# Kernel tuning notes

Hardware: AMD Instinct MI355X
Metric: run time of the kernel (lower is better)

The kernel has to match this reference:

```python
import math
import jax, jax.numpy as jnp
import numpy as np

NUM_HEADS = 16
TAU_RCS, LAMBDA_RCS = 2.0, 0.6
PATCH = 16
PREFIX = 8
GAUSS_STD = 5.0


def gaussian_window(d1, d2, std):
    c = 1.0 / (std * math.sqrt(2.0))
    k1 = (jnp.arange(d1, dtype=jnp.float32) - (d1 - 1) / 2.0) * c
    k2 = (jnp.arange(d2, dtype=jnp.float32) - (d2 - 1) / 2.0) * c
    return jnp.exp(-(k1[:, None] ** 2 + k2[None, :] ** 2))  # [d1, d2]


def attention_addition(d1, d2, prefix, std):
    # out[(a,b),(c,d)] = window[a-c+d1-1, b-d+d2-1]  (conv of delta images with window)
    win = gaussian_window(2 * d1 - 1, 2 * d2 - 1, std)
    ia = jnp.arange(d1)
    jb = jnp.arange(d2)
    r = ia[:, None] - ia[None, :] + (d1 - 1)   # [d1, d1]
    s = jb[:, None] - jb[None, :] + (d2 - 1)   # [d2, d2]
    add = win[r[:, None, :, None], s[None, :, None, :]]  # [d1,d2,d1,d2]
    add = add.reshape(d1 * d2, d1 * d2)
    add = jnp.pad(add, ((prefix, 0), (prefix, 0)))  # zero rows/cols for prefix tokens
    return add[None]  # [1, N, N]


def setup_inputs() -> dict:
    key = jax.random.key(0)
    ks = jax.random.split(key, 5)
    B, C = 4, 1024
    d1 = d2 = 512 // PATCH  # 32
    N = d1 * d2 + PREFIX    # 1032
    H = NUM_HEADS
    x = jax.random.normal(ks[0], (B, N, C), dtype=jnp.float32)
    qkv_w = jax.random.normal(ks[1], (3 * C, C), dtype=jnp.float32) * 0.02
    qkv_b = jnp.zeros((3 * C,), dtype=jnp.float32)
    proj_w = jax.random.normal(ks[2], (C, C), dtype=jnp.float32) * 0.02
    proj_b = jnp.zeros((C,), dtype=jnp.float32)
    attn_add = attention_addition(d1, d2, PREFIX, GAUSS_STD)
    # stored RCS attention maps are softmax outputs -> row-normalized positives
    rcs = jax.random.uniform(ks[3], (B * H, N, N), dtype=jnp.float32)
    rcs = rcs / jnp.sum(rcs, axis=-1, keepdims=True)
    return {"x": x, "qkv_w": qkv_w, "qkv_b": qkv_b, "proj_w": proj_w,
            "proj_b": proj_b, "attn_addition": attn_add, "rcs_attn": rcs}


def reference(x, qkv_w, qkv_b, proj_w, proj_b, attn_addition, rcs_attn):
    B, N, C = x.shape
    H = NUM_HEADS
    hd = C // H
    scale = hd ** -0.5
    qkv = jnp.einsum('bnc,dc->bnd', x, qkv_w) + qkv_b  # [B,N,3C]
    q, k, v = jnp.split(qkv, 3, axis=-1)
    def to_heads(t):
        return t.reshape(B, N, H, hd).transpose(0, 2, 1, 3).reshape(B * H, N, hd)
    k = to_heads(k)
    v = to_heads(v)
    # custom K-K attention with additive Gaussian bias
    attn = jnp.einsum('bnd,bmd->bnm', k, k) * scale + attn_addition
    attn = jax.nn.softmax(attn, axis=-1)
    # RCS blending with stored intermediate attention maps
    attn = TAU_RCS * ((1.0 - LAMBDA_RCS) * attn + LAMBDA_RCS * rcs_attn)
    out = jnp.einsum('bnm,bmd->bnd', attn, v)  # [B*H, N, hd]
    out = out.reshape(B, H, N, hd).transpose(0, 2, 1, 3).reshape(B, N, C)
    out = jnp.einsum('bnc,dc->bnd', out, proj_w) + proj_b
    return out
```

## Files before the change

kernel.cpp:

```cpp
#include <hip/hip_runtime.h>
#include <stdint.h>

#define NSEQ 1032
#define CDIM 1024
#define HD 64
#define H_HEADS 16
#define BROWS 4128
#define SCALE 0.125f

typedef __attribute__((ext_vector_type(8))) short bf16x8;
typedef __attribute__((ext_vector_type(4))) float f32x4;

__device__ __forceinline__ unsigned short f2bf(float f) {
  union { float f; uint32_t u; } c; c.f = f;
  uint32_t u = c.u;
  return (unsigned short)((u + 0x7fffu + ((u >> 16) & 1u)) >> 16);
}

__device__ __forceinline__ void gl16(const void* gp, void* lp) {
  __builtin_amdgcn_global_load_lds((const __attribute__((address_space(1))) void*)gp,
                                   (__attribute__((address_space(3))) void*)lp, 16, 0, 0);
}

__global__ void convert_f32_bf16(const float* __restrict__ src, unsigned short* __restrict__ dst, int n4) {
  int i = blockIdx.x * blockDim.x + threadIdx.x;
  if (i >= n4) return;
  float4 v = ((const float4*)src)[i];
  ushort4 o;
  o.x = f2bf(v.x); o.y = f2bf(v.y); o.z = f2bf(v.z); o.w = f2bf(v.w);
  ((ushort4*)dst)[i] = o;
}

template<int MODE>
__global__ __launch_bounds__(256, 2) void gemm_bt(
    const unsigned short* __restrict__ A,
    const unsigned short* __restrict__ Bw,
    const float* __restrict__ bias,
    unsigned short* __restrict__ outK,
    unsigned short* __restrict__ outV,
    float* __restrict__ outF,
    int M, int K)
{
  __shared__ unsigned short As[128 * 32];
  __shared__ unsigned short Bs[128 * 32];
  const int t = threadIdx.x;
  const int w = t >> 6, lane = t & 63, lr = lane & 15, lg = lane >> 4;
  const int wr = w >> 1, wc = w & 1;
  const int NXB = (MODE == 0) ? 16 : 8;
  const int cpx = gridDim.x >> 3;
  const int swz = (blockIdx.x & 7) * cpx + (blockIdx.x >> 3);
  const int m0 = (swz / NXB) * 128, n0 = (swz % NXB) * 128;
  f32x4 acc[4][4] = {};

  for (int ks = 0; ks < K; ks += 32) {
    #pragma unroll
    for (int q = 0; q < 2; ++q) {
      const int o = t + (q << 8);
      const int row = o >> 2, kc = o & 3;
      int ra = m0 + row; ra = ra < M ? ra : M - 1;
      gl16(A + (size_t)ra * K + ks + kc * 8, (void*)(As + o * 8));
      gl16(Bw + (size_t)(n0 + row) * K + ks + kc * 8, (void*)(Bs + o * 8));
    }
    __syncthreads();
    bf16x8 af[4], bfr[4];
    #pragma unroll
    for (int m = 0; m < 4; ++m)
      af[m] = *(const bf16x8*)(As + (wr * 64 + m * 16 + lr) * 32 + lg * 8);
    #pragma unroll
    for (int n = 0; n < 4; ++n)
      bfr[n] = *(const bf16x8*)(Bs + (wc * 64 + n * 16 + lr) * 32 + lg * 8);
    #pragma unroll
    for (int m = 0; m < 4; ++m)
      #pragma unroll
      for (int n = 0; n < 4; ++n)
        acc[m][n] = __builtin_amdgcn_mfma_f32_16x16x32_bf16(af[m], bfr[n], acc[m][n], 0, 0, 0);
    __syncthreads();
  }

  #pragma unroll
  for (int m = 0; m < 4; ++m) {
    const int rowb = m0 + wr * 64 + m * 16 + lg * 4;
    #pragma unroll
    for (int n = 0; n < 4; ++n) {
      const int col = n0 + wc * 64 + n * 16 + lr;
      const float bv = bias[col];
      #pragma unroll
      for (int r = 0; r < 4; ++r) {
        const int row = rowb + r;
        if (row >= M) continue;
        const float v = acc[m][n][r] + bv;
        if (MODE == 0) {
          const int b = row / NSEQ, nn = row - b * NSEQ;
          if (col < CDIM) {
            const int h = col >> 6, d = col & 63;
            outK[((size_t)(b * H_HEADS + h) * NSEQ + nn) * HD + d] = f2bf(v);
          } else {
            const int jj = col - CDIM, h = jj >> 6, d = jj & 63;
            outV[((size_t)(b * H_HEADS + h) * HD + d) * NSEQ + nn] = f2bf(v);
          }
        } else {
          outF[(size_t)row * CDIM + col] = v;
        }
      }
    }
  }
}

__global__ __launch_bounds__(256, 3) void attn_fused(
    const unsigned short* __restrict__ Kb,
    const unsigned short* __restrict__ Vt,
    const float* __restrict__ rcs,
    unsigned short* __restrict__ outp)
{
  __shared__ __align__(16) unsigned short Kc[2][64 * 64];
  __shared__ __align__(16) unsigned short Vs[2][64 * 64];
  __shared__ __align__(16) unsigned short Asm[64 * 72];
  __shared__ unsigned short Ps[64 * 72];
  const int t = threadIdx.x;
  const int w = t >> 6, lane = t & 63, lr = lane & 15, lg = lane >> 4;
  const int bid = blockIdx.x;
  const int nb = (bid & 7) * 136 + (bid >> 3);
  const int bh = nb / 17, rt = nb - bh * 17;
  const int i_base = rt * 64 + w * 16;
  const int arow = w * 16 + lr;
  const float* rbase = rcs + (size_t)bh * NSEQ * NSEQ;
  const unsigned short* kbase = Kb + (size_t)bh * NSEQ * HD;
  const unsigned short* vbase = Vt + (size_t)bh * HD * NSEQ;

  const unsigned short* srck[2]; int dok[2];
  const unsigned short* srcv[2]; int dov[2];
  #pragma unroll
  for (int q = 0; q < 2; ++q) {
    const int p = t + (q << 8);
    const int row = p >> 3, sch = p & 7;
    const int gch = (sch ^ row) & 7;
    srck[q] = kbase + (size_t)row * HD + gch * 8;  dok[q] = p * 8;
    srcv[q] = vbase + (size_t)row * NSEQ + gch * 8; dov[q] = p * 8;
  }
  auto stage_kv = [&](int tB, int buf) {
    #pragma unroll
    for (int q = 0; q < 2; ++q) gl16(srck[q] + (size_t)tB * HD, (void*)(Kc[buf] + dok[q]));
    #pragma unroll
    for (int q = 0; q < 2; ++q) gl16(srcv[q] + tB, (void*)(Vs[buf] + dov[q]));
  };
  auto stage_kv_tail = [&](int buf) {
    const int tB = 1024;
    #pragma unroll
    for (int q = 0; q < 2; ++q) {
      const int p = t + (q << 8);
      const int row = p >> 3, sch = p & 7;
      const int gch = (sch ^ row) & 7;
      int mrow = tB + row; if (mrow > NSEQ - 1) mrow = NSEQ - 1;
      gl16(kbase + (size_t)mrow * HD + gch * 8, (void*)(Kc[buf] + p * 8));
    }
    #pragma unroll
    for (int q = 0; q < 2; ++q) {
      const int p = t + (q << 8);
      const int row = p >> 3, sch = p & 7;
      const int gch = (sch ^ row) & 7;
      int gc = tB + gch * 8; if (gc > NSEQ - 8) gc = NSEQ - 8;
      gl16(vbase + (size_t)row * NSEQ + gc, (void*)(Vs[buf] + p * 8));
    }
  };

  const int ccol = (lane & 15) * 4;
  const float* rsrc[4]; int lrow_loc[4];
  #pragma unroll
  for (int j = 0; j < 4; ++j) {
    lrow_loc[j] = w * 16 + j * 4 + (lane >> 4);
    int grow = rt * 64 + lrow_loc[j]; if (grow > NSEQ - 1) grow = NSEQ - 1;
    rsrc[j] = rbase + (size_t)grow * NSEQ;
  }
  f32x4 rreg[4];
  auto ld_rcs = [&](int tB) {
    int gcol = tB + ccol; if (gcol > NSEQ - 4) gcol = NSEQ - 4;
    #pragma unroll
    for (int j = 0; j < 4; ++j) rreg[j] = *(const f32x4*)(rsrc[j] + gcol);
  };
  auto wr_rcs = [&]() {
    #pragma unroll
    for (int j = 0; j < 4; ++j) {
      ushort4 o;
      o.x = f2bf(rreg[j][0]); o.y = f2bf(rreg[j][1]);
      o.z = f2bf(rreg[j][2]); o.w = f2bf(rreg[j][3]);
      *(ushort4*)(Asm + lrow_loc[j] * 72 + ccol) = o;
    }
  };

  bf16x8 akr[2];
  {
    int row = i_base + lr; if (row > NSEQ - 1) row = NSEQ - 1;
    const unsigned short* p = kbase + (size_t)row * HD + lg * 8;
    akr[0] = *(const bf16x8*)(p);
    akr[1] = *(const bf16x8*)(p + 32);
  }

  const int irow_base = i_base + lg * 4;
  float u[16], v[16];
  #pragma unroll
  for (int fn = 0; fn < 4; ++fn) {
    const int x = 16 * fn + lr;
    const int m1_0 = ((x + 24) >> 5) - 1;
    const int m2 = (x - 8) & 31;
    #pragma unroll
    for (int r = 0; r < 4; ++r) {
      const int irow = irow_base + r;
      const int ip = irow - 8;
      const int i1 = ip >> 5, j1 = ip & 31;
      const int di = i1 - m1_0, dj = j1 - m2;
      const float iok = (irow >= 8) ? 1.f : 0.f;
      u[fn * 4 + r] = __expf(-0.02f * (float)(di * di + dj * dj)) * iok;
      v[fn * 4 + r] = __expf(0.08f * (float)di);
    }
  }
  const float C1 = 0.92311634639f;
  const float C2 = 0.85214378896f;

  f32x4 accP[4] = {};
  f32x4 accR[4] = {};
  float lsum[4] = {0.f, 0.f, 0.f, 0.f};

  ld_rcs(0);
  stage_kv(0, 0);
  wr_rcs();
  asm volatile("s_waitcnt vmcnt(0)");
  __builtin_amdgcn_s_barrier();
  __builtin_amdgcn_sched_barrier(0);

  for (int mt = 0; mt < 17; ++mt) {
    const int mB = mt * 64;
    const int cur = mt & 1, nxt = cur ^ 1;

    if (mt < 16)       ld_rcs(mB + 64);
    if (mt < 15)       stage_kv(mB + 64, nxt);
    else if (mt == 15) stage_kv_tail(nxt);

    const unsigned short* kc = Kc[cur];
    const unsigned short* vsb = Vs[cur];

    __builtin_amdgcn_s_setprio(1);
    f32x4 s[4];
    #pragma unroll
    for (int fn = 0; fn < 4; ++fn) {
      const int row = 16 * fn + lr;
      const int r7 = row & 7;
      f32x4 z = {0.f, 0.f, 0.f, 0.f};
      bf16x8 b0 = *(const bf16x8*)(kc + row * 64 + ((lg ^ r7) & 7) * 8);
      bf16x8 b1 = *(const bf16x8*)(kc + row * 64 + (((4 + lg) ^ r7) & 7) * 8);
      z = __builtin_amdgcn_mfma_f32_16x16x32_bf16(akr[0], b0, z, 0, 0, 0);
      z = __builtin_amdgcn_mfma_f32_16x16x32_bf16(akr[1], b1, z, 0, 0, 0);
      s[fn] = z;
    }
    __builtin_amdgcn_s_setprio(0);

    #pragma unroll
    for (int fn = 0; fn < 4; ++fn) {
      const int mcol = mB + 16 * fn + lr;
      const float mok = (mcol >= 8 && mcol < NSEQ) ? 1.f : 0.f;
      const bool mlt = (mcol < NSEQ);
      #pragma unroll
      for (int r = 0; r < 4; ++r) {
        const int fi = fn * 4 + r;
        const float sv = s[fn][r] * SCALE + u[fi] * mok;
        const float p = mlt ? __expf(sv) : 0.f;
        lsum[r] += p;
        Ps[(w * 16 + lg * 4 + r) * 72 + 16 * fn + lr] = f2bf(p);
        u[fi] *= v[fi] * C1;
        v[fi] *= C2;
      }
    }

    bf16x8 af[2];
    #pragma unroll
    for (int kf = 0; kf < 2; ++kf) {
      const int kg = mB + kf * 32 + lg * 8;
      if (kg + 8 <= NSEQ) {
        af[kf] = *(const bf16x8*)(Asm + arow * 72 + kf * 32 + lg * 8);
      } else {
        #pragma unroll
        for (int j = 0; j < 8; ++j) af[kf][j] = 0;
      }
    }

    bf16x8 pa0 = *(const bf16x8*)(Ps + (w * 16 + lr) * 72 + lg * 8);
    bf16x8 pa1 = *(const bf16x8*)(Ps + (w * 16 + lr) * 72 + 32 + lg * 8);
    __builtin_amdgcn_s_setprio(1);
    #pragma unroll
    for (int fd = 0; fd < 4; ++fd) {
      const int row = 16 * fd + lr;
      const int r7 = row & 7;
      bf16x8 v0 = *(const bf16x8*)(vsb + row * 64 + ((lg ^ r7) & 7) * 8);
      bf16x8 v1 = *(const bf16x8*)(vsb + row * 64 + (((4 + lg) ^ r7) & 7) * 8);
      accP[fd] = __builtin_amdgcn_mfma_f32_16x16x32_bf16(pa0, v0, accP[fd], 0, 0, 0);
      accP[fd] = __builtin_amdgcn_mfma_f32_16x16x32_bf16(pa1, v1, accP[fd], 0, 0, 0);
      accR[fd] = __builtin_amdgcn_mfma_f32_16x16x32_bf16(af[0], v0, accR[fd], 0, 0, 0);
      accR[fd] = __builtin_amdgcn_mfma_f32_16x16x32_bf16(af[1], v1, accR[fd], 0, 0, 0);
    }
    __builtin_amdgcn_s_setprio(0);

    if (mt < 16) wr_rcs();

    __builtin_amdgcn_sched_barrier(0);
    asm volatile("s_waitcnt vmcnt(0)");
    __builtin_amdgcn_s_barrier();
    __builtin_amdgcn_sched_barrier(0);
  }

  #pragma unroll
  for (int r = 0; r < 4; ++r) {
    float vv = lsum[r];
    vv += __shfl_xor(vv, 1); vv += __shfl_xor(vv, 2);
    vv += __shfl_xor(vv, 4); vv += __shfl_xor(vv, 8);
    lsum[r] = vv;
  }

  const int b = bh >> 4, hh = bh & 15;
  #pragma unroll
  for (int fd = 0; fd < 4; ++fd) {
    #pragma unroll
    for (int r = 0; r < 4; ++r) {
      const int irow = i_base + lg * 4 + r;
      if (irow < NSEQ) {
        const float val = 0.8f * accP[fd][r] / lsum[r] + 1.2f * accR[fd][r];
        outp[(size_t)(b * NSEQ + irow) * CDIM + hh * 64 + 16 * fd + lr] = f2bf(val);
      }
    }
  }
}

extern "C" void kernel_launch(void* const* d_in, const int* in_sizes, int n_in,
                              void* d_out, int out_size, void* d_ws, size_t ws_size,
                              hipStream_t stream) {
  (void)in_sizes; (void)n_in; (void)out_size; (void)ws_size;
  const float* x      = (const float*)d_in[0];
  const float* qkv_w  = (const float*)d_in[1];
  const float* qkv_b  = (const float*)d_in[2];
  const float* proj_w = (const float*)d_in[3];
  const float* proj_b = (const float*)d_in[4];
  const float* rcs    = (const float*)d_in[6];
  float* out = (float*)d_out;

  char* ws = (char*)d_ws;
  unsigned short* x_bf = (unsigned short*)ws; ws += (size_t)BROWS * CDIM * 2;
  unsigned short* wkv  = (unsigned short*)ws; ws += (size_t)2048 * CDIM * 2;
  unsigned short* wp   = (unsigned short*)ws; ws += (size_t)1024 * CDIM * 2;
  unsigned short* Kb   = (unsigned short*)ws; ws += (size_t)64 * NSEQ * HD * 2;
  unsigned short* Vt   = (unsigned short*)ws; ws += (size_t)64 * HD * NSEQ * 2;
  unsigned short* op   = (unsigned short*)ws; ws += (size_t)BROWS * CDIM * 2;

  const int n1 = BROWS * CDIM / 4, n2 = 2048 * CDIM / 4, n3 = 1024 * CDIM / 4;
  convert_f32_bf16<<<(n1 + 255) / 256, 256, 0, stream>>>(x, x_bf, n1);
  convert_f32_bf16<<<(n2 + 255) / 256, 256, 0, stream>>>(qkv_w + 1024 * 1024, wkv, n2);
  convert_f32_bf16<<<(n3 + 255) / 256, 256, 0, stream>>>(proj_w, wp, n3);

  gemm_bt<0><<<528, 256, 0, stream>>>(x_bf, wkv, qkv_b + 1024, Kb, Vt, nullptr, BROWS, CDIM);
  attn_fused<<<1088, 256, 0, stream>>>(Kb, Vt, rcs, op);
  gemm_bt<1><<<264, 256, 0, stream>>>(op, wp, proj_b, nullptr, nullptr, out, BROWS, CDIM);
}
```

Measured before the change: 180.8 us.

## Double attention row tile to 128 rows with 512-thread blocks

The attention kernel now processes 128 query rows per block using 8 waves instead of 64 rows with 4 waves, so each K/V tile staged in shared memory is reused by twice as many rows. This halves the total K/V global traffic and the staging work per row. In exchange, blocks are larger with more shared memory (bigger Asm/Ps buffers), occupancy bounds change to 2 blocks of 512 threads, and the last row tile is mostly padding (9 tiles of 128 cover 1032 rows).

```diff
diff --git a/kernel.cpp b/kernel.cpp
--- a/kernel.cpp
+++ b/kernel.cpp
@@ -106,7 +106,7 @@
   }
 }
 
-__global__ __launch_bounds__(256, 3) void attn_fused(
+__global__ __launch_bounds__(512, 2) void attn_fused(
     const unsigned short* __restrict__ Kb,
     const unsigned short* __restrict__ Vt,
     const float* __restrict__ rcs,
@@ -114,53 +114,39 @@
 {
   __shared__ __align__(16) unsigned short Kc[2][64 * 64];
   __shared__ __align__(16) unsigned short Vs[2][64 * 64];
-  __shared__ __align__(16) unsigned short Asm[64 * 72];
-  __shared__ unsigned short Ps[64 * 72];
+  __shared__ __align__(16) unsigned short Asm[128 * 72];
+  __shared__ unsigned short Ps[128 * 72];
   const int t = threadIdx.x;
   const int w = t >> 6, lane = t & 63, lr = lane & 15, lg = lane >> 4;
   const int bid = blockIdx.x;
-  const int nb = (bid & 7) * 136 + (bid >> 3);
-  const int bh = nb / 17, rt = nb - bh * 17;
-  const int i_base = rt * 64 + w * 16;
+  const int nb = (bid & 7) * 72 + (bid >> 3);
+  const int bh = nb / 9, rt = nb - bh * 9;
+  const int i_base = rt * 128 + w * 16;
   const int arow = w * 16 + lr;
   const float* rbase = rcs + (size_t)bh * NSEQ * NSEQ;
   const unsigned short* kbase = Kb + (size_t)bh * NSEQ * HD;
   const unsigned short* vbase = Vt + (size_t)bh * HD * NSEQ;
 
-  const unsigned short* srck[2]; int dok[2];
-  const unsigned short* srcv[2]; int dov[2];
-  #pragma unroll
-  for (int q = 0; q < 2; ++q) {
-    const int p = t + (q << 8);
-    const int row = p >> 3, sch = p & 7;
+  const unsigned short* srck1; int dok1;
+  const unsigned short* srcv1; int dov1;
+  {
+    const int row = t >> 3, sch = t & 7;
     const int gch = (sch ^ row) & 7;
-    srck[q] = kbase + (size_t)row * HD + gch * 8;  dok[q] = p * 8;
-    srcv[q] = vbase + (size_t)row * NSEQ + gch * 8; dov[q] = p * 8;
+    srck1 = kbase + (size_t)row * HD + gch * 8;   dok1 = t * 8;
+    srcv1 = vbase + (size_t)row * NSEQ + gch * 8; dov1 = t * 8;
   }
   auto stage_kv = [&](int tB, int buf) {
-    #pragma unroll
-    for (int q = 0; q < 2; ++q) gl16(srck[q] + (size_t)tB * HD, (void*)(Kc[buf] + dok[q]));
-    #pragma unroll
-    for (int q = 0; q < 2; ++q) gl16(srcv[q] + tB, (void*)(Vs[buf] + dov[q]));
+    gl16(srck1 + (size_t)tB * HD, (void*)(Kc[buf] + dok1));
+    gl16(srcv1 + tB, (void*)(Vs[buf] + dov1));
   };
   auto stage_kv_tail = [&](int buf) {
     const int tB = 1024;
-    #pragma unroll
-    for (int q = 0; q < 2; ++q) {
-      const int p = t + (q << 8);
-      const int row = p >> 3, sch = p & 7;
-      const int gch = (sch ^ row) & 7;
-      int mrow = tB + row; if (mrow > NSEQ - 1) mrow = NSEQ - 1;
-      gl16(kbase + (size_t)mrow * HD + gch * 8, (void*)(Kc[buf] + p * 8));
-    }
-    #pragma unroll
-    for (int q = 0; q < 2; ++q) {
-      const int p = t + (q << 8);
-      const int row = p >> 3, sch = p & 7;
-      const int gch = (sch ^ row) & 7;
-      int gc = tB + gch * 8; if (gc > NSEQ - 8) gc = NSEQ - 8;
-      gl16(vbase + (size_t)row * NSEQ + gc, (void*)(Vs[buf] + p * 8));
-    }
+    const int row = t >> 3, sch = t & 7;
+    const int gch = (sch ^ row) & 7;
+    int mrow = tB + row; if (mrow > NSEQ - 1) mrow = NSEQ - 1;
+    gl16(kbase + (size_t)mrow * HD + gch * 8, (void*)(Kc[buf] + t * 8));
+    int gc = tB + gch * 8; if (gc > NSEQ - 8) gc = NSEQ - 8;
+    gl16(vbase + (size_t)row * NSEQ + gc, (void*)(Vs[buf] + t * 8));
   };
 
   const int ccol = (lane & 15) * 4;
@@ -168,7 +154,7 @@
   #pragma unroll
   for (int j = 0; j < 4; ++j) {
     lrow_loc[j] = w * 16 + j * 4 + (lane >> 4);
-    int grow = rt * 64 + lrow_loc[j]; if (grow > NSEQ - 1) grow = NSEQ - 1;
+    int grow = rt * 128 + lrow_loc[j]; if (grow > NSEQ - 1) grow = NSEQ - 1;
     rsrc[j] = rbase + (size_t)grow * NSEQ;
   }
   f32x4 rreg[4];
@@ -354,6 +340,6 @@
   convert_f32_bf16<<<(n3 + 255) / 256, 256, 0, stream>>>(proj_w, wp, n3);
 
   gemm_bt<0><<<528, 256, 0, stream>>>(x_bf, wkv, qkv_b + 1024, Kb, Vt, nullptr, BROWS, CDIM);
-  attn_fused<<<1088, 256, 0, stream>>>(Kb, Vt, rcs, op);
+  attn_fused<<<576, 512, 0, stream>>>(Kb, Vt, rcs, op);
   gemm_bt<1><<<264, 256, 0, stream>>>(op, wp, proj_b, nullptr, nullptr, out, BROWS, CDIM);
 }
```

Result: slower. 221.5 us (+22.5%).

## Prefetch RCS tiles two steps ahead with double-banked registers

Applied to the files above, without the earlier changes.

The fused attention loop now keeps two register banks for the RCS map. Each iteration loads the fp32 tile two steps ahead while converting and writing the previously loaded bank to LDS. The end-of-iteration wait becomes a partial vmcnt(4), so the newest RCS loads can stay in flight across the barrier, where the old code drained every outstanding load. This is meant to hide more of the global memory latency of the large RCS stream, at the cost of 16 extra VGPRs per thread, which could cause spills or lower occupancy under the launch bound.

```diff
diff --git a/kernel.cpp b/kernel.cpp
--- a/kernel.cpp
+++ b/kernel.cpp
@@ -106,6 +106,98 @@
   }
 }
 
+#define LD_RCS(tB, rr) do {                                              \
+    int gcol_ = (tB) + ccol; if (gcol_ > NSEQ - 4) gcol_ = NSEQ - 4;     \
+    _Pragma("unroll")                                                    \
+    for (int j = 0; j < 4; ++j) rr[j] = *(const f32x4*)(rsrc[j] + gcol_); \
+  } while (0)
+
+#define WR_RCS(rr) do {                                                  \
+    _Pragma("unroll")                                                    \
+    for (int j = 0; j < 4; ++j) {                                        \
+      ushort4 o_;                                                        \
+      o_.x = f2bf(rr[j][0]); o_.y = f2bf(rr[j][1]);                      \
+      o_.z = f2bf(rr[j][2]); o_.w = f2bf(rr[j][3]);                      \
+      *(ushort4*)(Asm + lrow_loc[j] * 72 + ccol) = o_;                   \
+    }                                                                    \
+  } while (0)
+
+#define ATTN_STEP(MT, LDBANK, WRBANK, DO_BARRIER) do {                   \
+    const int mB_ = (MT) * 64;                                           \
+    const int cur_ = (MT) & 1, nxt_ = cur_ ^ 1;                          \
+    if ((MT) < 15)       stage_kv(mB_ + 64, nxt_);                       \
+    else if ((MT) == 15) stage_kv_tail(nxt_);                            \
+    __builtin_amdgcn_sched_barrier(0);                                   \
+    if ((MT) < 15) { LD_RCS(mB_ + 128, LDBANK); }                        \
+    __builtin_amdgcn_sched_barrier(0);                                   \
+    const unsigned short* kc_ = Kc[cur_];                                \
+    const unsigned short* vsb_ = Vs[cur_];                               \
+    __builtin_amdgcn_s_setprio(1);                                       \
+    f32x4 s_[4];                                                         \
+    _Pragma("unroll")                                                    \
+    for (int fn = 0; fn < 4; ++fn) {                                     \
+      const int row_ = 16 * fn + lr;                                     \
+      const int r7_ = row_ & 7;                                          \
+      f32x4 z_ = {0.f, 0.f, 0.f, 0.f};                                   \
+      bf16x8 b0_ = *(const bf16x8*)(kc_ + row_ * 64 + ((lg ^ r7_) & 7) * 8); \
+      bf16x8 b1_ = *(const bf16x8*)(kc_ + row_ * 64 + (((4 + lg) ^ r7_) & 7) * 8); \
+      z_ = __builtin_amdgcn_mfma_f32_16x16x32_bf16(akr[0], b0_, z_, 0, 0, 0); \
+      z_ = __builtin_amdgcn_mfma_f32_16x16x32_bf16(akr[1], b1_, z_, 0, 0, 0); \
+      s_[fn] = z_;                                                       \
+    }                                                                    \
+    __builtin_amdgcn_s_setprio(0);                                       \
+    _Pragma("unroll")                                                    \
+    for (int fn = 0; fn < 4; ++fn) {                                     \
+      const int mcol_ = mB_ + 16 * fn + lr;                              \
+      const float mok_ = (mcol_ >= 8 && mcol_ < NSEQ) ? 1.f : 0.f;       \
+      const bool mlt_ = (mcol_ < NSEQ);                                  \
+      _Pragma("unroll")                                                  \
+      for (int r = 0; r < 4; ++r) {                                      \
+        const int fi_ = fn * 4 + r;                                      \
+        const float sv_ = s_[fn][r] * SCALE + u[fi_] * mok_;             \
+        const float p_ = mlt_ ? __expf(sv_) : 0.f;                       \
+        lsum[r] += p_;                                                   \
+        Ps[(w * 16 + lg * 4 + r) * 72 + 16 * fn + lr] = f2bf(p_);        \
+        u[fi_] *= v[fi_] * C1;                                           \
+        v[fi_] *= C2;                                                    \
+      }                                                                  \
+    }                                                                    \
+    bf16x8 af_[2];                                                       \
+    _Pragma("unroll")                                                    \
+    for (int kf = 0; kf < 2; ++kf) {                                     \
+      const int kg_ = mB_ + kf * 32 + lg * 8;                            \
+      if (kg_ + 8 <= NSEQ) {                                             \
+        af_[kf] = *(const bf16x8*)(Asm + arow * 72 + kf * 32 + lg * 8);  \
+      } else {                                                           \
+        _Pragma("unroll")                                                \
+        for (int j = 0; j < 8; ++j) af_[kf][j] = 0;                      \
+      }                                                                  \
+    }                                                                    \
+    bf16x8 pa0_ = *(const bf16x8*)(Ps + (w * 16 + lr) * 72 + lg * 8);    \
+    bf16x8 pa1_ = *(const bf16x8*)(Ps + (w * 16 + lr) * 72 + 32 + lg * 8); \
+    __builtin_amdgcn_s_setprio(1);                                       \
+    _Pragma("unroll")                                                    \
+    for (int fd = 0; fd < 4; ++fd) {                                     \
+      const int row_ = 16 * fd + lr;                                     \
+      const int r7_ = row_ & 7;                                          \
+      bf16x8 v0_ = *(const bf16x8*)(vsb_ + row_ * 64 + ((lg ^ r7_) & 7) * 8); \
+      bf16x8 v1_ = *(const bf16x8*)(vsb_ + row_ * 64 + (((4 + lg) ^ r7_) & 7) * 8); \
+      accP[fd] = __builtin_amdgcn_mfma_f32_16x16x32_bf16(pa0_, v0_, accP[fd], 0, 0, 0); \
+      accP[fd] = __builtin_amdgcn_mfma_f32_16x16x32_bf16(pa1_, v1_, accP[fd], 0, 0, 0); \
+      accR[fd] = __builtin_amdgcn_mfma_f32_16x16x32_bf16(af_[0], v0_, accR[fd], 0, 0, 0); \
+      accR[fd] = __builtin_amdgcn_mfma_f32_16x16x32_bf16(af_[1], v1_, accR[fd], 0, 0, 0); \
+    }                                                                    \
+    __builtin_amdgcn_s_setprio(0);                                       \
+    if ((MT) < 16) { WR_RCS(WRBANK); }                                   \
+    __builtin_amdgcn_sched_barrier(0);                                   \
+    if ((MT) < 15) { asm volatile("s_waitcnt vmcnt(4)"); }               \
+    else           { asm volatile("s_waitcnt vmcnt(0)"); }               \
+    if (DO_BARRIER) {                                                    \
+      __builtin_amdgcn_s_barrier();                                      \
+      __builtin_amdgcn_sched_barrier(0);                                 \
+    }                                                                    \
+  } while (0)
+
 __global__ __launch_bounds__(256, 3) void attn_fused(
     const unsigned short* __restrict__ Kb,
     const unsigned short* __restrict__ Vt,
@@ -171,21 +263,7 @@
     int grow = rt * 64 + lrow_loc[j]; if (grow > NSEQ - 1) grow = NSEQ - 1;
     rsrc[j] = rbase + (size_t)grow * NSEQ;
   }
-  f32x4 rreg[4];
-  auto ld_rcs = [&](int tB) {
-    int gcol = tB + ccol; if (gcol > NSEQ - 4) gcol = NSEQ - 4;
-    #pragma unroll
-    for (int j = 0; j < 4; ++j) rreg[j] = *(const f32x4*)(rsrc[j] + gcol);
-  };
-  auto wr_rcs = [&]() {
-    #pragma unroll
-    for (int j = 0; j < 4; ++j) {
-      ushort4 o;
-      o.x = f2bf(rreg[j][0]); o.y = f2bf(rreg[j][1]);
-      o.z = f2bf(rreg[j][2]); o.w = f2bf(rreg[j][3]);
-      *(ushort4*)(Asm + lrow_loc[j] * 72 + ccol) = o;
-    }
-  };
+  f32x4 rregA[4], rregB[4];
 
   bf16x8 akr[2];
   {
@@ -220,91 +298,19 @@
   f32x4 accR[4] = {};
   float lsum[4] = {0.f, 0.f, 0.f, 0.f};
 
-  ld_rcs(0);
   stage_kv(0, 0);
-  wr_rcs();
-  asm volatile("s_waitcnt vmcnt(0)");
+  LD_RCS(0, rregA);
+  WR_RCS(rregA);
+  LD_RCS(64, rregB);
+  asm volatile("s_waitcnt vmcnt(4)");
   __builtin_amdgcn_s_barrier();
   __builtin_amdgcn_sched_barrier(0);
 
-  for (int mt = 0; mt < 17; ++mt) {
-    const int mB = mt * 64;
-    const int cur = mt & 1, nxt = cur ^ 1;
-
-    if (mt < 16)       ld_rcs(mB + 64);
-    if (mt < 15)       stage_kv(mB + 64, nxt);
-    else if (mt == 15) stage_kv_tail(nxt);
-
-    const unsigned short* kc = Kc[cur];
-    const unsigned short* vsb = Vs[cur];
-
-    __builtin_amdgcn_s_setprio(1);
-    f32x4 s[4];
-    #pragma unroll
-    for (int fn = 0; fn < 4; ++fn) {
-      const int row = 16 * fn + lr;
-      const int r7 = row & 7;
-      f32x4 z = {0.f, 0.f, 0.f, 0.f};
-      bf16x8 b0 = *(const bf16x8*)(kc + row * 64 + ((lg ^ r7) & 7) * 8);
-      bf16x8 b1 = *(const bf16x8*)(kc + row * 64 + (((4 + lg) ^ r7) & 7) * 8);
-      z = __builtin_amdgcn_mfma_f32_16x16x32_bf16(akr[0], b0, z, 0, 0, 0);
-      z = __builtin_amdgcn_mfma_f32_16x16x32_bf16(akr[1], b1, z, 0, 0, 0);
-      s[fn] = z;
-    }
-    __builtin_amdgcn_s_setprio(0);
-
-    #pragma unroll
-    for (int fn = 0; fn < 4; ++fn) {
-      const int mcol = mB + 16 * fn + lr;
-      const float mok = (mcol >= 8 && mcol < NSEQ) ? 1.f : 0.f;
-      const bool mlt = (mcol < NSEQ);
-      #pragma unroll
-      for (int r = 0; r < 4; ++r) {
-        const int fi = fn * 4 + r;
-        const float sv = s[fn][r] * SCALE + u[fi] * mok;
-        const float p = mlt ? __expf(sv) : 0.f;
-        lsum[r] += p;
-        Ps[(w * 16 + lg * 4 + r) * 72 + 16 * fn + lr] = f2bf(p);
-        u[fi] *= v[fi] * C1;
-        v[fi] *= C2;
-      }
-    }
-
-    bf16x8 af[2];
-    #pragma unroll
-    for (int kf = 0; kf < 2; ++kf) {
-      const int kg = mB + kf * 32 + lg * 8;
-      if (kg + 8 <= NSEQ) {
-        af[kf] = *(const bf16x8*)(Asm + arow * 72 + kf * 32 + lg * 8);
-      } else {
-        #pragma unroll
-        for (int j = 0; j < 8; ++j) af[kf][j] = 0;
-      }
-    }
-
-    bf16x8 pa0 = *(const bf16x8*)(Ps + (w * 16 + lr) * 72 + lg * 8);
-    bf16x8 pa1 = *(const bf16x8*)(Ps + (w * 16 + lr) * 72 + 32 + lg * 8);
-    __builtin_amdgcn_s_setprio(1);
-    #pragma unroll
-    for (int fd = 0; fd < 4; ++fd) {
-      const int row = 16 * fd + lr;
-      const int r7 = row & 7;
-      bf16x8 v0 = *(const bf16x8*)(vsb + row * 64 + ((lg ^ r7) & 7) * 8);
-      bf16x8 v1 = *(const bf16x8*)(vsb + row * 64 + (((4 + lg) ^ r7) & 7) * 8);
-      accP[fd] = __builtin_amdgcn_mfma_f32_16x16x32_bf16(pa0, v0, accP[fd], 0, 0, 0);
-      accP[fd] = __builtin_amdgcn_mfma_f32_16x16x32_bf16(pa1, v1, accP[fd], 0, 0, 0);
-      accR[fd] = __builtin_amdgcn_mfma_f32_16x16x32_bf16(af[0], v0, accR[fd], 0, 0, 0);
-      accR[fd] = __builtin_amdgcn_mfma_f32_16x16x32_bf16(af[1], v1, accR[fd], 0, 0, 0);
-    }
-    __builtin_amdgcn_s_setprio(0);
-
-    if (mt < 16) wr_rcs();
-
-    __builtin_amdgcn_sched_barrier(0);
-    asm volatile("s_waitcnt vmcnt(0)");
-    __builtin_amdgcn_s_barrier();
-    __builtin_amdgcn_sched_barrier(0);
-  }
+  for (int pp = 0; pp < 8; ++pp) {
+    ATTN_STEP(2 * pp,     rregA, rregB, 1);
+    ATTN_STEP(2 * pp + 1, rregB, rregA, 1);
+  }
+  ATTN_STEP(16, rregA, rregB, 0);
 
   #pragma unroll
   for (int r = 0; r < 4; ++r) {
```

Measured after the change: 353.9 us. 95.7% more time.

## Process two 64-row query tiles per block to reuse staged K/V

Applied to the files above, without the earlier changes.

Each attention block now handles 128 rows (two 64-row sub-tiles) instead of 64, so every K/V tile staged into shared memory feeds twice as many MFMAs. The grid shrinks from 1088 to 576 blocks and the occupancy hint drops from 3 to 2 blocks per CU. The Gaussian bias recurrence for the second tile is derived from the first tile's state with a constant factor, which saves registers. The aim is to cut K/V staging traffic and barrier overhead per row, at the cost of more registers and LDS per block and fewer resident waves. The rcs stream, which is probably the dominant cost, is unchanged.

```diff
diff --git a/kernel.cpp b/kernel.cpp
--- a/kernel.cpp
+++ b/kernel.cpp
@@ -106,7 +106,7 @@
   }
 }
 
-__global__ __launch_bounds__(256, 3) void attn_fused(
+__global__ __launch_bounds__(256, 2) void attn_fused(
     const unsigned short* __restrict__ Kb,
     const unsigned short* __restrict__ Vt,
     const float* __restrict__ rcs,
@@ -114,15 +114,17 @@
 {
   __shared__ __align__(16) unsigned short Kc[2][64 * 64];
   __shared__ __align__(16) unsigned short Vs[2][64 * 64];
-  __shared__ __align__(16) unsigned short Asm[64 * 72];
-  __shared__ unsigned short Ps[64 * 72];
+  __shared__ __align__(16) unsigned short Asm[128 * 72];
+  __shared__ unsigned short Ps[128 * 72];
   const int t = threadIdx.x;
   const int w = t >> 6, lane = t & 63, lr = lane & 15, lg = lane >> 4;
   const int bid = blockIdx.x;
-  const int nb = (bid & 7) * 136 + (bid >> 3);
-  const int bh = nb / 17, rt = nb - bh * 17;
-  const int i_base = rt * 64 + w * 16;
-  const int arow = w * 16 + lr;
+  const int nb = (bid & 7) * 72 + (bid >> 3);
+  const int bh = nb / 9, rt = nb - bh * 9;
+  const int iA = rt * 128 + w * 16;
+  const int iB = iA + 64;
+  const int laA = w * 16;
+  const int laB = 64 + w * 16;
   const float* rbase = rcs + (size_t)bh * NSEQ * NSEQ;
   const unsigned short* kbase = Kb + (size_t)bh * NSEQ * HD;
   const unsigned short* vbase = Vt + (size_t)bh * HD * NSEQ;
@@ -164,39 +166,51 @@
   };
 
   const int ccol = (lane & 15) * 4;
-  const float* rsrc[4]; int lrow_loc[4];
+  const int jrow = (lane >> 4);
+  const float* rsrcA[4]; const float* rsrcB[4];
   #pragma unroll
   for (int j = 0; j < 4; ++j) {
-    lrow_loc[j] = w * 16 + j * 4 + (lane >> 4);
-    int grow = rt * 64 + lrow_loc[j]; if (grow > NSEQ - 1) grow = NSEQ - 1;
-    rsrc[j] = rbase + (size_t)grow * NSEQ;
-  }
-  f32x4 rreg[4];
+    int gA = rt * 128 + laA + j * 4 + jrow; if (gA > NSEQ - 1) gA = NSEQ - 1;
+    int gB = rt * 128 + laB + j * 4 + jrow; if (gB > NSEQ - 1) gB = NSEQ - 1;
+    rsrcA[j] = rbase + (size_t)gA * NSEQ;
+    rsrcB[j] = rbase + (size_t)gB * NSEQ;
+  }
+  f32x4 rgA[4], rgB[4];
   auto ld_rcs = [&](int tB) {
     int gcol = tB + ccol; if (gcol > NSEQ - 4) gcol = NSEQ - 4;
     #pragma unroll
-    for (int j = 0; j < 4; ++j) rreg[j] = *(const f32x4*)(rsrc[j] + gcol);
+    for (int j = 0; j < 4; ++j) rgA[j] = *(const f32x4*)(rsrcA[j] + gcol);
+    #pragma unroll
+    for (int j = 0; j < 4; ++j) rgB[j] = *(const f32x4*)(rsrcB[j] + gcol);
   };
   auto wr_rcs = [&]() {
     #pragma unroll
     for (int j = 0; j < 4; ++j) {
       ushort4 o;
-      o.x = f2bf(rreg[j][0]); o.y = f2bf(rreg[j][1]);
-      o.z = f2bf(rreg[j][2]); o.w = f2bf(rreg[j][3]);
-      *(ushort4*)(Asm + lrow_loc[j] * 72 + ccol) = o;
+      o.x = f2bf(rgA[j][0]); o.y = f2bf(rgA[j][1]);
+      o.z = f2bf(rgA[j][2]); o.w = f2bf(rgA[j][3]);
+      *(ushort4*)(Asm + (laA + j * 4 + jrow) * 72 + ccol) = o;
+    }
+    #pragma unroll
+    for (int j = 0; j < 4; ++j) {
+      ushort4 o;
+      o.x = f2bf(rgB[j][0]); o.y = f2bf(rgB[j][1]);
+      o.z = f2bf(rgB[j][2]); o.w = f2bf(rgB[j][3]);
+      *(ushort4*)(Asm + (laB + j * 4 + jrow) * 72 + ccol) = o;
     }
   };
 
-  bf16x8 akr[2];
+  bf16x8 akrA[2], akrB[2];
   {
-    int row = i_base + lr; if (row > NSEQ - 1) row = NSEQ - 1;
-    const unsigned short* p = kbase + (size_t)row * HD + lg * 8;
-    akr[0] = *(const bf16x8*)(p);
-    akr[1] = *(const bf16x8*)(p + 32);
-  }
-
-  const int irow_base = i_base + lg * 4;
-  float u[16], v[16];
+    int rowA = iA + lr; if (rowA > NSEQ - 1) rowA = NSEQ - 1;
+    int rowB = iB + lr; if (rowB > NSEQ - 1) rowB = NSEQ - 1;
+    const unsigned short* pA = kbase + (size_t)rowA * HD + lg * 8;
+    const unsigned short* pB = kbase + (size_t)rowB * HD + lg * 8;
+    akrA[0] = *(const bf16x8*)(pA);  akrA[1] = *(const bf16x8*)(pA + 32);
+    akrB[0] = *(const bf16x8*)(pB);  akrB[1] = *(const bf16x8*)(pB + 32);
+  }
+
+  float uA[16], vA[16], uB[16];
   #pragma unroll
   for (int fn = 0; fn < 4; ++fn) {
     const int x = 16 * fn + lr;
@@ -204,21 +218,29 @@
     const int m2 = (x - 8) & 31;
     #pragma unroll
     for (int r = 0; r < 4; ++r) {
-      const int irow = irow_base + r;
-      const int ip = irow - 8;
-      const int i1 = ip >> 5, j1 = ip & 31;
-      const int di = i1 - m1_0, dj = j1 - m2;
-      const float iok = (irow >= 8) ? 1.f : 0.f;
-      u[fn * 4 + r] = __expf(-0.02f * (float)(di * di + dj * dj)) * iok;
-      v[fn * 4 + r] = __expf(0.08f * (float)di);
+      const int irA = iA + lg * 4 + r;
+      const int ipA = irA - 8;
+      const int i1A = ipA >> 5, j1A = ipA & 31;
+      const int diA = i1A - m1_0, djA = j1A - m2;
+      const float iokA = (irA >= 8) ? 1.f : 0.f;
+      uA[fn * 4 + r] = __expf(-0.02f * (float)(diA * diA + djA * djA)) * iokA;
+      vA[fn * 4 + r] = __expf(0.08f * (float)diA);
+      const int irB = iB + lg * 4 + r;
+      const int ipB = irB - 8;
+      const int i1B = ipB >> 5, j1B = ipB & 31;
+      const int diB = i1B - m1_0, djB = j1B - m2;
+      const float iokB = (irB >= 8) ? 1.f : 0.f;
+      uB[fn * 4 + r] = __expf(-0.02f * (float)(diB * diB + djB * djB)) * iokB;
     }
   }
   const float C1 = 0.92311634639f;
   const float C2 = 0.85214378896f;
-
-  f32x4 accP[4] = {};
-  f32x4 accR[4] = {};
-  float lsum[4] = {0.f, 0.f, 0.f, 0.f};
+  const float E008 = 1.08328706767f;
+
+  f32x4 accPA[4] = {}, accRA[4] = {};
+  f32x4 accPB[4] = {}, accRB[4] = {};
+  float lsA[4] = {0.f, 0.f, 0.f, 0.f};
+  float lsB[4] = {0.f, 0.f, 0.f, 0.f};
 
   ld_rcs(0);
   stage_kv(0, 0);
@@ -239,17 +261,21 @@
     const unsigned short* vsb = Vs[cur];
 
     __builtin_amdgcn_s_setprio(1);
-    f32x4 s[4];
+    f32x4 sA[4], sB[4];
     #pragma unroll
     for (int fn = 0; fn < 4; ++fn) {
       const int row = 16 * fn + lr;
       const int r7 = row & 7;
-      f32x4 z = {0.f, 0.f, 0.f, 0.f};
       bf16x8 b0 = *(const bf16x8*)(kc + row * 64 + ((lg ^ r7) & 7) * 8);
       bf16x8 b1 = *(const bf16x8*)(kc + row * 64 + (((4 + lg) ^ r7) & 7) * 8);
-      z = __builtin_amdgcn_mfma_f32_16x16x32_bf16(akr[0], b0, z, 0, 0, 0);
-      z = __builtin_amdgcn_mfma_f32_16x16x32_bf16(akr[1], b1, z, 0, 0, 0);
-      s[fn] = z;
+      f32x4 zA = {0.f, 0.f, 0.f, 0.f};
+      zA = __builtin_amdgcn_mfma_f32_16x16x32_bf16(akrA[0], b0, zA, 0, 0, 0);
+      zA = __builtin_amdgcn_mfma_f32_16x16x32_bf16(akrA[1], b1, zA, 0, 0, 0);
+      sA[fn] = zA;
+      f32x4 zB = {0.f, 0.f, 0.f, 0.f};
+      zB = __builtin_amdgcn_mfma_f32_16x16x32_bf16(akrB[0], b0, zB, 0, 0, 0);
+      zB = __builtin_amdgcn_mfma_f32_16x16x32_bf16(akrB[1], b1, zB, 0, 0, 0);
+      sB[fn] = zB;
     }
     __builtin_amdgcn_s_setprio(0);
 
@@ -261,29 +287,37 @@
       #pragma unroll
       for (int r = 0; r < 4; ++r) {
         const int fi = fn * 4 + r;
-        const float sv = s[fn][r] * SCALE + u[fi] * mok;
-        const float p = mlt ? __expf(sv) : 0.f;
-        lsum[r] += p;
-        Ps[(w * 16 + lg * 4 + r) * 72 + 16 * fn + lr] = f2bf(p);
-        u[fi] *= v[fi] * C1;
-        v[fi] *= C2;
+        const float svA = sA[fn][r] * SCALE + uA[fi] * mok;
+        const float pA = mlt ? __expf(svA) : 0.f;
+        lsA[r] += pA;
+        Ps[(laA + lg * 4 + r) * 72 + 16 * fn + lr] = f2bf(pA);
+        const float svB = sB[fn][r] * SCALE + uB[fi] * mok;
+        const float pB = mlt ? __expf(svB) : 0.f;
+        lsB[r] += pB;
+        Ps[(laB + lg * 4 + r) * 72 + 16 * fn + lr] = f2bf(pB);
+        uB[fi] *= vA[fi] * E008;
+        uA[fi] *= vA[fi] * C1;
+        vA[fi] *= C2;
       }
     }
 
-    bf16x8 af[2];
+    bf16x8 afA[2], afB[2];
     #pragma unroll
     for (int kf = 0; kf < 2; ++kf) {
       const int kg = mB + kf * 32 + lg * 8;
       if (kg + 8 <= NSEQ) {
-        af[kf] = *(const bf16x8*)(Asm + arow * 72 + kf * 32 + lg * 8);
+        afA[kf] = *(const bf16x8*)(Asm + (laA + lr) * 72 + kf * 32 + lg * 8);
+        afB[kf] = *(const bf16x8*)(Asm + (laB + lr) * 72 + kf * 32 + lg * 8);
       } else {
         #pragma unroll
-        for (int j = 0; j < 8; ++j) af[kf][j] = 0;
+        for (int j = 0; j < 8; ++j) { afA[kf][j] = 0; afB[kf][j] = 0; }
       }
     }
 
-    bf16x8 pa0 = *(const bf16x8*)(Ps + (w * 16 + lr) * 72 + lg * 8);
-    bf16x8 pa1 = *(const bf16x8*)(Ps + (w * 16 + lr) * 72 + 32 + lg * 8);
+    bf16x8 paA0 = *(const bf16x8*)(Ps + (laA + lr) * 72 + lg * 8);
+    bf16x8 paA1 = *(const bf16x8*)(Ps + (laA + lr) * 72 + 32 + lg * 8);
+    bf16x8 paB0 = *(const bf16x8*)(Ps + (laB + lr) * 72 + lg * 8);
+    bf16x8 paB1 = *(const bf16x8*)(Ps + (laB + lr) * 72 + 32 + lg * 8);
     __builtin_amdgcn_s_setprio(1);
     #pragma unroll
     for (int fd = 0; fd < 4; ++fd) {
@@ -291,10 +325,14 @@
       const int r7 = row & 7;
       bf16x8 v0 = *(const bf16x8*)(vsb + row * 64 + ((lg ^ r7) & 7) * 8);
       bf16x8 v1 = *(const bf16x8*)(vsb + row * 64 + (((4 + lg) ^ r7) & 7) * 8);
-      accP[fd] = __builtin_amdgcn_mfma_f32_16x16x32_bf16(pa0, v0, accP[fd], 0, 0, 0);
-      accP[fd] = __builtin_amdgcn_mfma_f32_16x16x32_bf16(pa1, v1, accP[fd], 0, 0, 0);
-      accR[fd] = __builtin_amdgcn_mfma_f32_16x16x32_bf16(af[0], v0, accR[fd], 0, 0, 0);
-      accR[fd] = __builtin_amdgcn_mfma_f32_16x16x32_bf16(af[1], v1, accR[fd], 0, 0, 0);
+      accPA[fd] = __builtin_amdgcn_mfma_f32_16x16x32_bf16(paA0, v0, accPA[fd], 0, 0, 0);
+      accPA[fd] = __builtin_amdgcn_mfma_f32_16x16x32_bf16(paA1, v1, accPA[fd], 0, 0, 0);
+      accRA[fd] = __builtin_amdgcn_mfma_f32_16x16x32_bf16(afA[0], v0, accRA[fd], 0, 0, 0);
+      accRA[fd] = __builtin_amdgcn_mfma_f32_16x16x32_bf16(afA[1], v1, accRA[fd], 0, 0, 0);
+      accPB[fd] = __builtin_amdgcn_mfma_f32_16x16x32_bf16(paB0, v0, accPB[fd], 0, 0, 0);
+      accPB[fd] = __builtin_amdgcn_mfma_f32_16x16x32_bf16(paB1, v1, accPB[fd], 0, 0, 0);
+      accRB[fd] = __builtin_amdgcn_mfma_f32_16x16x32_bf16(afB[0], v0, accRB[fd], 0, 0, 0);
+      accRB[fd] = __builtin_amdgcn_mfma_f32_16x16x32_bf16(afB[1], v1, accRB[fd], 0, 0, 0);
     }
     __builtin_amdgcn_s_setprio(0);
 
@@ -308,10 +346,14 @@
 
   #pragma unroll
   for (int r = 0; r < 4; ++r) {
-    float vv = lsum[r];
-    vv += __shfl_xor(vv, 1); vv += __shfl_xor(vv, 2);
-    vv += __shfl_xor(vv, 4); vv += __shfl_xor(vv, 8);
-    lsum[r] = vv;
+    float a = lsA[r];
+    a += __shfl_xor(a, 1); a += __shfl_xor(a, 2);
+    a += __shfl_xor(a, 4); a += __shfl_xor(a, 8);
+    lsA[r] = a;
+    float b2 = lsB[r];
+    b2 += __shfl_xor(b2, 1); b2 += __shfl_xor(b2, 2);
+    b2 += __shfl_xor(b2, 4); b2 += __shfl_xor(b2, 8);
+    lsB[r] = b2;
   }
 
   const int b = bh >> 4, hh = bh & 15;
@@ -319,10 +361,15 @@
   for (int fd = 0; fd < 4; ++fd) {
     #pragma unroll
     for (int r = 0; r < 4; ++r) {
-      const int irow = i_base + lg * 4 + r;
-      if (irow < NSEQ) {
-        const float val = 0.8f * accP[fd][r] / lsum[r] + 1.2f * accR[fd][r];
-        outp[(size_t)(b * NSEQ + irow) * CDIM + hh * 64 + 16 * fd + lr] = f2bf(val);
+      const int irA = iA + lg * 4 + r;
+      if (irA < NSEQ) {
+        const float val = 0.8f * accPA[fd][r] / lsA[r] + 1.2f * accRA[fd][r];
+        outp[(size_t)(b * NSEQ + irA) * CDIM + hh * 64 + 16 * fd + lr] = f2bf(val);
+      }
+      const int irB = iB + lg * 4 + r;
+      if (irB < NSEQ) {
+        const float val = 0.8f * accPB[fd][r] / lsB[r] + 1.2f * accRB[fd][r];
+        outp[(size_t)(b * NSEQ + irB) * CDIM + hh * 64 + 16 * fd + lr] = f2bf(val);
       }
     }
   }
@@ -354,6 +401,6 @@
   convert_f32_bf16<<<(n3 + 255) / 256, 256, 0, stream>>>(proj_w, wp, n3);
 
   gemm_bt<0><<<528, 256, 0, stream>>>(x_bf, wkv, qkv_b + 1024, Kb, Vt, nullptr, BROWS, CDIM);
-  attn_fused<<<1088, 256, 0, stream>>>(Kb, Vt, rcs, op);
+  attn_fused<<<576, 256, 0, stream>>>(Kb, Vt, rcs, op);
   gemm_bt<1><<<264, 256, 0, stream>>>(op, wp, proj_b, nullptr, nullptr, out, BROWS, CDIM);
 }
```

Result: slower. 315.1 us (+74.2%).
